# Kernel optimization log

Measured on AMD Instinct MI355X. Metric: run time of the kernel, lower is better.

## Reference

```python
import jax, jax.numpy as jnp
import numpy as np

N = 50000
E = 800000
D_IN = 128
D_OUT = 128


def setup_inputs() -> dict:
    key = jax.random.key(0)
    ks = jax.random.split(key, 12)
    x = jax.random.normal(ks[0], (N, D_IN), dtype=jnp.float32)
    W1 = jax.random.normal(ks[1], (D_IN, D_OUT), dtype=jnp.float32) * (1.0 / np.sqrt(D_IN))
    b1 = jnp.zeros((D_OUT,), dtype=jnp.float32)
    W2 = jax.random.normal(ks[2], (D_IN, D_OUT), dtype=jnp.float32) * (1.0 / np.sqrt(D_IN))
    b2 = jnp.zeros((D_OUT,), dtype=jnp.float32)
    # inverted-dropout masks, p=0.5 -> values in {0, 2}
    def mask(k):
        return jnp.where(jax.random.uniform(k, (N, D_IN)) < 0.5, 0.0, 2.0).astype(jnp.float32)
    mask_pos1 = mask(ks[3])
    mask_neg1 = mask(ks[4])
    mask_pos2 = mask(ks[5])
    mask_neg2 = mask(ks[6])
    edge_index1 = jax.random.randint(ks[7], (2, E), 0, N, dtype=jnp.int32)
    edge_index2 = jax.random.randint(ks[8], (2, E), 0, N, dtype=jnp.int32)
    perm1 = jax.random.permutation(ks[9], N).astype(jnp.int32)
    perm2 = jax.random.permutation(ks[10], N).astype(jnp.int32)
    return dict(x=x, W1=W1, b1=b1, W2=W2, b2=b2,
                mask_pos1=mask_pos1, mask_neg1=mask_neg1,
                mask_pos2=mask_pos2, mask_neg2=mask_neg2,
                edge_index1=edge_index1, edge_index2=edge_index2,
                perm1=perm1, perm2=perm2)


def gcn_conv(x, W, b, edge_index):
    """PyG GCNConv: add self-loops, symmetric normalization, then x@W aggregation + bias."""
    n = x.shape[0]
    xw = x @ W  # [N, D_OUT]
    loops = jnp.arange(n, dtype=edge_index.dtype)
    src = jnp.concatenate([edge_index[0], loops])
    dst = jnp.concatenate([edge_index[1], loops])
    deg = jax.ops.segment_sum(jnp.ones_like(dst, dtype=xw.dtype), dst, num_segments=n)
    dinv = jax.lax.rsqrt(jnp.maximum(deg, 1.0))  # deg >= 1 due to self-loops
    norm = dinv[src] * dinv[dst]                 # [E+N]
    msg = xw[src] * norm[:, None]                # [E+N, D_OUT]
    out = jax.ops.segment_sum(msg, dst, num_segments=n)
    return out + b


def _branch(x, W, b, edge_index, mask_pos, mask_neg, perm):
    pos_h = jax.nn.relu(gcn_conv(x * mask_pos, W, b, edge_index))
    neg_in = (x * mask_neg)[perm]
    neg_h = jax.nn.relu(gcn_conv(neg_in, W, b, edge_index))
    summary = jnp.mean(pos_h, axis=0, keepdims=True)  # [1, D_OUT]
    return pos_h, neg_h, summary


def reference(x, W1, b1, W2, b2, mask_pos1, mask_neg1, mask_pos2, mask_neg2,
              edge_index1, edge_index2, perm1, perm2):
    p1, n1, s1 = _branch(x, W1, b1, edge_index1, mask_pos1, mask_neg1, perm1)
    p2, n2, s2 = _branch(x, W2, b2, edge_index2, mask_pos2, mask_neg2, perm2)
    return (p1, n1, s1, p2, n2, s2)
```

## Files before the change

### kernel.cpp

```cpp
#include <hip/hip_runtime.h>
#include <hip/hip_fp16.h>

#define NN 50000
#define NE 800000
#define D 128
#define NB 196
#define FILL_BLOCKS 1024
#define GEMM_BLOCKS 3128
#define RNG 6250
#define ESL 6250

typedef _Float16 half8_t __attribute__((ext_vector_type(8)));
typedef _Float16 half4_t __attribute__((ext_vector_type(4)));
typedef float f32x4 __attribute__((ext_vector_type(4)));

__global__ void k_init(int* cnt1, int* cnt2, float* s1, float* s2) {
    int i = blockIdx.x * blockDim.x + threadIdx.x;
    int stride = gridDim.x * blockDim.x;
    for (int j = i; j < NN; j += stride) { cnt1[j] = 0; cnt2[j] = 0; }
    if (i < D) { s1[i] = 0.f; s2[i] = 0.f; }
}

__global__ void k_count(const int* __restrict__ dst1, const int* __restrict__ dst2,
                        int* cnt1, int* cnt2) {
    int r = blockIdx.x & 7;
    int rank = blockIdx.x >> 3;
    unsigned lo = r * RNG;
    int base = rank * ESL;
    for (int e = base + threadIdx.x; e < base + ESL; e += 256) {
        int d1 = dst1[e];
        if ((unsigned)(d1 - lo) < RNG) atomicAdd(&cnt1[d1], 1);
        int d2 = dst2[e];
        if ((unsigned)(d2 - lo) < RNG) atomicAdd(&cnt2[d2], 1);
    }
}

__global__ void k_part(const int* __restrict__ cnt1, const int* __restrict__ cnt2,
                       int* part1, int* part2) {
    __shared__ int sm1[256], sm2[256];
    int t = threadIdx.x;
    int idx = blockIdx.x * 256 + t;
    int v1 = (idx < NN) ? cnt1[idx] : 0;
    int v2 = (idx < NN) ? cnt2[idx] : 0;
    sm1[t] = v1; sm2[t] = v2;
    __syncthreads();
    for (int off = 128; off > 0; off >>= 1) {
        if (t < off) { sm1[t] += sm1[t + off]; sm2[t] += sm2[t + off]; }
        __syncthreads();
    }
    if (t == 0) { part1[blockIdx.x] = sm1[0]; part2[blockIdx.x] = sm2[0]; }
}

__global__ void k_scanp(int* part1, int* part2) {
    __shared__ int sm1[256], sm2[256];
    int t = threadIdx.x;
    int v1 = (t < NB) ? part1[t] : 0;
    int v2 = (t < NB) ? part2[t] : 0;
    sm1[t] = v1; sm2[t] = v2;
    __syncthreads();
    for (int off = 1; off < 256; off <<= 1) {
        int a1 = (t >= off) ? sm1[t - off] : 0;
        int a2 = (t >= off) ? sm2[t - off] : 0;
        __syncthreads();
        sm1[t] += a1; sm2[t] += a2;
        __syncthreads();
    }
    if (t < NB) { part1[t] = sm1[t] - v1; part2[t] = sm2[t] - v2; }
}

__global__ void k_apply(const int* __restrict__ cnt1, const int* __restrict__ cnt2,
                        const int* __restrict__ part1, const int* __restrict__ part2,
                        int* rp1, int* rp2, int* cur1, int* cur2,
                        float* dinv1, float* dinv2) {
    __shared__ int sm1[256], sm2[256];
    int b = blockIdx.x, t = threadIdx.x;
    int idx = b * 256 + t;
    int v1 = (idx < NN) ? cnt1[idx] : 0;
    int v2 = (idx < NN) ? cnt2[idx] : 0;
    sm1[t] = v1; sm2[t] = v2;
    __syncthreads();
    for (int off = 1; off < 256; off <<= 1) {
        int a1 = (t >= off) ? sm1[t - off] : 0;
        int a2 = (t >= off) ? sm2[t - off] : 0;
        __syncthreads();
        sm1[t] += a1; sm2[t] += a2;
        __syncthreads();
    }
    int e1 = sm1[t] - v1 + part1[b];
    int e2 = sm2[t] - v2 + part2[b];
    if (idx < NN) {
        rp1[idx] = e1; cur1[idx] = e1; dinv1[idx] = rsqrtf((float)(v1 + 1));
        rp2[idx] = e2; cur2[idx] = e2; dinv2[idx] = rsqrtf((float)(v2 + 1));
    } else if (idx == NN) {
        rp1[NN] = e1; rp2[NN] = e2;
    }
}

__launch_bounds__(256)
__global__ void k_fill_gemm(const int* __restrict__ src1, const int* __restrict__ dst1,
                            const int* __restrict__ src2, const int* __restrict__ dst2,
                            int* cur1, int* cur2, int* col1, int* col2,
                            const float* __restrict__ x,
                            const float* __restrict__ W1, const float* __restrict__ W2,
                            const float* __restrict__ mp1, const float* __restrict__ mn1,
                            const float* __restrict__ mp2, const float* __restrict__ mn2,
                            const int* __restrict__ perm1, const int* __restrict__ perm2,
                            const float* __restrict__ dinv1, const float* __restrict__ dinv2,
                            _Float16* xwi1, _Float16* xwi2) {
    __shared__ __align__(16) _Float16 WT[128][136];
    int t = threadIdx.x;

    if (blockIdx.x < FILL_BLOCKS) {
        int r = blockIdx.x & 7;
        int rank = blockIdx.x >> 3;
        unsigned lo = r * RNG;
        int base = rank * ESL;
        for (int e = base + t; e < base + ESL; e += 256) {
            int d1 = dst1[e];
            if ((unsigned)(d1 - lo) < RNG) {
                int p = atomicAdd(&cur1[d1], 1);
                col1[p] = src1[e];
            }
            int d2 = dst2[e];
            if ((unsigned)(d2 - lo) < RNG) {
                int p = atomicAdd(&cur2[d2], 1);
                col2[p] = src2[e];
            }
        }
        return;
    }

    int g = blockIdx.x - FILL_BLOCKS;
    int which = g / 782;
    int bx = g - which * 782;
    const float* W = (which < 2) ? W1 : W2;
    const float* mask = (which == 0) ? mp1 : (which == 1) ? mn1 : (which == 2) ? mp2 : mn2;
    const int* perm = (which == 1) ? perm1 : (which == 3) ? perm2 : nullptr;
    const float* dinv = (which < 2) ? dinv1 : dinv2;
    _Float16* out = ((which < 2) ? xwi1 : xwi2) + ((which & 1) ? 128 : 0);

    for (int i = 0; i < 16; i++) {
        int idx = i * 256 + t;
        int k = idx >> 5;
        int j4 = (idx & 31) * 4;
        float4 w = ((const float4*)W)[idx];
        WT[j4 + 0][k] = (_Float16)w.x;
        WT[j4 + 1][k] = (_Float16)w.y;
        WT[j4 + 2][k] = (_Float16)w.z;
        WT[j4 + 3][k] = (_Float16)w.w;
    }
    __syncthreads();

    int wave = t >> 6;
    int lane = t & 63;
    int quad = lane >> 4;
    int m = lane & 15;
    int tile = bx * 4 + wave;
    if (tile * 16 >= NN) return;

    int row = tile * 16 + m;
    int grow = perm ? perm[row] : row;
    const float* xrow = x + (long)grow * D;
    const float* mrow = mask + (long)grow * D;

    half8_t a[4];
    for (int kk = 0; kk < 4; kk++) {
        int k0 = kk * 32 + quad * 8;
        float4 xa = *(const float4*)(xrow + k0);
        float4 xb = *(const float4*)(xrow + k0 + 4);
        float4 ma = *(const float4*)(mrow + k0);
        float4 mb = *(const float4*)(mrow + k0 + 4);
        a[kk][0] = (_Float16)(xa.x * ma.x);
        a[kk][1] = (_Float16)(xa.y * ma.y);
        a[kk][2] = (_Float16)(xa.z * ma.z);
        a[kk][3] = (_Float16)(xa.w * ma.w);
        a[kk][4] = (_Float16)(xb.x * mb.x);
        a[kk][5] = (_Float16)(xb.y * mb.y);
        a[kk][6] = (_Float16)(xb.z * mb.z);
        a[kk][7] = (_Float16)(xb.w * mb.w);
    }

    int rbase = tile * 16 + quad * 4;
    float ds0 = dinv[rbase + 0], ds1 = dinv[rbase + 1];
    float ds2 = dinv[rbase + 2], ds3 = dinv[rbase + 3];

    for (int nt = 0; nt < 8; nt++) {
        f32x4 acc = {0.f, 0.f, 0.f, 0.f};
        for (int kk = 0; kk < 4; kk++) {
            half8_t b = *(const half8_t*)(&WT[nt * 16 + m][kk * 32 + quad * 8]);
            acc = __builtin_amdgcn_mfma_f32_16x16x32_f16(a[kk], b, acc, 0, 0, 0);
        }
        int n = nt * 16 + m;
        out[(long)(rbase + 0) * 256 + n] = (_Float16)(acc[0] * ds0);
        out[(long)(rbase + 1) * 256 + n] = (_Float16)(acc[1] * ds1);
        out[(long)(rbase + 2) * 256 + n] = (_Float16)(acc[2] * ds2);
        out[(long)(rbase + 3) * 256 + n] = (_Float16)(acc[3] * ds3);
    }
}

__launch_bounds__(256)
__global__ void k_agg(const _Float16* __restrict__ xwi1, const _Float16* __restrict__ xwi2,
                      const int* __restrict__ rp1, const int* __restrict__ col1,
                      const float* __restrict__ dinv1,
                      const int* __restrict__ rp2, const int* __restrict__ col2,
                      const float* __restrict__ dinv2,
                      const float* __restrict__ b1, const float* __restrict__ b2,
                      float* out) {
    int g = blockIdx.y;
    const _Float16* xwi = g ? xwi2 : xwi1;
    const int* rp = g ? rp2 : rp1;
    const int* col = g ? col2 : col1;
    const float* dinv = g ? dinv2 : dinv1;
    const float* bias = g ? b2 : b1;
    float* pos_out = out + (g ? 12800128L : 0L);
    float* neg_out = out + (g ? 19200128L : 6400000L);

    int t = threadIdx.x;
    int wave = t >> 6, lane = t & 63;
    int i = blockIdx.x * 4 + wave;
    if (i >= NN) return;
    int j4 = lane * 4;

    half4_t sv = *(const half4_t*)(xwi + (long)i * 256 + j4);
    float a0 = (float)sv[0], a1 = (float)sv[1], a2 = (float)sv[2], a3 = (float)sv[3];
    int e0 = rp[i], e1 = rp[i + 1];
    int e = e0;
    for (; e + 8 <= e1; e += 8) {
        int s0 = col[e + 0], s1 = col[e + 1], s2 = col[e + 2], s3 = col[e + 3];
        int s4 = col[e + 4], s5 = col[e + 5], s6 = col[e + 6], s7 = col[e + 7];
        half4_t v0 = *(const half4_t*)(xwi + (long)s0 * 256 + j4);
        half4_t v1 = *(const half4_t*)(xwi + (long)s1 * 256 + j4);
        half4_t v2 = *(const half4_t*)(xwi + (long)s2 * 256 + j4);
        half4_t v3 = *(const half4_t*)(xwi + (long)s3 * 256 + j4);
        half4_t v4 = *(const half4_t*)(xwi + (long)s4 * 256 + j4);
        half4_t v5 = *(const half4_t*)(xwi + (long)s5 * 256 + j4);
        half4_t v6 = *(const half4_t*)(xwi + (long)s6 * 256 + j4);
        half4_t v7 = *(const half4_t*)(xwi + (long)s7 * 256 + j4);
        a0 += (float)v0[0] + (float)v1[0] + (float)v2[0] + (float)v3[0]
            + (float)v4[0] + (float)v5[0] + (float)v6[0] + (float)v7[0];
        a1 += (float)v0[1] + (float)v1[1] + (float)v2[1] + (float)v3[1]
            + (float)v4[1] + (float)v5[1] + (float)v6[1] + (float)v7[1];
        a2 += (float)v0[2] + (float)v1[2] + (float)v2[2] + (float)v3[2]
            + (float)v4[2] + (float)v5[2] + (float)v6[2] + (float)v7[2];
        a3 += (float)v0[3] + (float)v1[3] + (float)v2[3] + (float)v3[3]
            + (float)v4[3] + (float)v5[3] + (float)v6[3] + (float)v7[3];
    }
    for (; e + 4 <= e1; e += 4) {
        int s0 = col[e + 0], s1 = col[e + 1], s2 = col[e + 2], s3 = col[e + 3];
        half4_t v0 = *(const half4_t*)(xwi + (long)s0 * 256 + j4);
        half4_t v1 = *(const half4_t*)(xwi + (long)s1 * 256 + j4);
        half4_t v2 = *(const half4_t*)(xwi + (long)s2 * 256 + j4);
        half4_t v3 = *(const half4_t*)(xwi + (long)s3 * 256 + j4);
        a0 += (float)v0[0] + (float)v1[0] + (float)v2[0] + (float)v3[0];
        a1 += (float)v0[1] + (float)v1[1] + (float)v2[1] + (float)v3[1];
        a2 += (float)v0[2] + (float)v1[2] + (float)v2[2] + (float)v3[2];
        a3 += (float)v0[3] + (float)v1[3] + (float)v2[3] + (float)v3[3];
    }
    for (; e < e1; e++) {
        int s = col[e];
        half4_t v = *(const half4_t*)(xwi + (long)s * 256 + j4);
        a0 += (float)v[0]; a1 += (float)v[1]; a2 += (float)v[2]; a3 += (float)v[3];
    }
    float di = dinv[i];
    int jj = (lane < 32) ? j4 : (j4 - 128);
    const f32x4* bp = (const f32x4*)(bias + jj);
    f32x4 bv = *bp;
    f32x4 o;
    o[0] = fmaxf(0.f, di * a0 + bv[0]);
    o[1] = fmaxf(0.f, di * a1 + bv[1]);
    o[2] = fmaxf(0.f, di * a2 + bv[2]);
    o[3] = fmaxf(0.f, di * a3 + bv[3]);
    float* dst = ((lane < 32) ? pos_out : neg_out) + (long)i * D + jj;
    __builtin_nontemporal_store(o, (f32x4*)dst);
}

__launch_bounds__(256)
__global__ void k_sum(const float* __restrict__ pos1, const float* __restrict__ pos2,
                      float* s1, float* s2) {
    int g = blockIdx.y;
    const float* pos = g ? pos2 : pos1;
    float* s = g ? s2 : s1;
    int t = threadIdx.x;
    int rg = t >> 5;
    int j = (t & 31) * 4;
    float4 acc = {0.f, 0.f, 0.f, 0.f};
    for (int i = blockIdx.x * 8 + rg; i < NN; i += gridDim.x * 8) {
        float4 v = *(const float4*)(pos + (long)i * D + j);
        acc.x += v.x; acc.y += v.y; acc.z += v.z; acc.w += v.w;
    }
    __shared__ float sm[8][128];
    sm[rg][j + 0] = acc.x;
    sm[rg][j + 1] = acc.y;
    sm[rg][j + 2] = acc.z;
    sm[rg][j + 3] = acc.w;
    __syncthreads();
    if (t < 128) {
        float v = 0.f;
        for (int r = 0; r < 8; r++) v += sm[r][t];
        atomicAdd(&s[t], v * (1.0f / NN));
    }
}

extern "C" void kernel_launch(void* const* d_in, const int* in_sizes, int n_in,
                              void* d_out, int out_size, void* d_ws, size_t ws_size,
                              hipStream_t stream) {
    const float* x   = (const float*)d_in[0];
    const float* W1  = (const float*)d_in[1];
    const float* b1  = (const float*)d_in[2];
    const float* W2  = (const float*)d_in[3];
    const float* b2  = (const float*)d_in[4];
    const float* mp1 = (const float*)d_in[5];
    const float* mn1 = (const float*)d_in[6];
    const float* mp2 = (const float*)d_in[7];
    const float* mn2 = (const float*)d_in[8];
    const int* e1 = (const int*)d_in[9];
    const int* e2 = (const int*)d_in[10];
    const int* perm1 = (const int*)d_in[11];
    const int* perm2 = (const int*)d_in[12];
    const int* src1 = e1;       const int* dst1 = e1 + NE;
    const int* src2 = e2;       const int* dst2 = e2 + NE;
    float* out = (float*)d_out;

    char* w = (char*)d_ws;
    _Float16* xwi1 = (_Float16*)w; w += (size_t)NN * 256 * 2;
    _Float16* xwi2 = (_Float16*)w; w += (size_t)NN * 256 * 2;
    int* cnt1 = (int*)w;  w += (size_t)NN * 4;
    int* cnt2 = (int*)w;  w += (size_t)NN * 4;
    int* cur1 = (int*)w;  w += (size_t)NN * 4;
    int* cur2 = (int*)w;  w += (size_t)NN * 4;
    int* rp1 = (int*)w;   w += (size_t)(NN + 4) * 4;
    int* rp2 = (int*)w;   w += (size_t)(NN + 4) * 4;
    int* col1 = (int*)w;  w += (size_t)NE * 4;
    int* col2 = (int*)w;  w += (size_t)NE * 4;
    float* dinv1 = (float*)w; w += (size_t)NN * 4;
    float* dinv2 = (float*)w; w += (size_t)NN * 4;
    int* part1 = (int*)w; w += (size_t)256 * 4;
    int* part2 = (int*)w; w += (size_t)256 * 4;

    float* s1 = out + 12800000L;
    float* s2 = out + 25600128L;
    const float* pos1 = out;
    const float* pos2 = out + 12800128L;

    k_init<<<dim3(256), 256, 0, stream>>>(cnt1, cnt2, s1, s2);
    k_count<<<dim3(1024), 256, 0, stream>>>(dst1, dst2, cnt1, cnt2);
    k_part<<<dim3(NB), 256, 0, stream>>>(cnt1, cnt2, part1, part2);
    k_scanp<<<dim3(1), 256, 0, stream>>>(part1, part2);
    k_apply<<<dim3(NB), 256, 0, stream>>>(cnt1, cnt2, part1, part2,
                                          rp1, rp2, cur1, cur2, dinv1, dinv2);
    k_fill_gemm<<<dim3(FILL_BLOCKS + GEMM_BLOCKS), 256, 0, stream>>>(
        src1, dst1, src2, dst2, cur1, cur2, col1, col2,
        x, W1, W2, mp1, mn1, mp2, mn2, perm1, perm2, dinv1, dinv2, xwi1, xwi2);
    k_agg<<<dim3(12500, 2), 256, 0, stream>>>(xwi1, xwi2,
                                              rp1, col1, dinv1, rp2, col2, dinv2,
                                              b1, b2, out);
    k_sum<<<dim3(128, 2), 256, 0, stream>>>(pos1, pos2, s1, s2);
}
```

Measured before the change: 531.7 us.

## Interleave fill and GEMM blocks; stage GEMM output via LDS for coalesced stores

The fused fill/GEMM kernel now interleaves CSR-fill blocks with GEMM blocks in groups of eight, so the atomic-heavy scatter work overlaps with MFMA work instead of running as a front-loaded phase. The GEMM swaps MFMA operands so each lane holds a row-major output fragment. Results are scaled by dinv, written to shared memory, and then stored to global memory as 16-byte vectors instead of scattered 2-byte stores. The W transpose load is also reworked to write half8 vectors into LDS. This adds an extra __syncthreads and keeps eight accumulator vectors live in registers, which raises register pressure.

```diff
diff --git a/kernel.cpp b/kernel.cpp
--- a/kernel.cpp
+++ b/kernel.cpp
@@ -5,8 +5,7 @@
 #define NE 800000
 #define D 128
 #define NB 196
-#define FILL_BLOCKS 1024
-#define GEMM_BLOCKS 3128
+#define TOT_BLOCKS 4152
 #define RNG 6250
 #define ESL 6250
 
@@ -109,10 +108,12 @@
                             _Float16* xwi1, _Float16* xwi2) {
     __shared__ __align__(16) _Float16 WT[128][136];
     int t = threadIdx.x;
-
-    if (blockIdx.x < FILL_BLOCKS) {
-        int r = blockIdx.x & 7;
-        int rank = blockIdx.x >> 3;
+    int bid = blockIdx.x;
+    int grp = bid >> 3;
+
+    if (((grp & 3) == 0) && (grp < 512)) {
+        int r = bid & 7;
+        int rank = grp >> 2;
         unsigned lo = r * RNG;
         int base = rank * ESL;
         for (int e = base + t; e < base + ESL; e += 256) {
@@ -130,7 +131,7 @@
         return;
     }
 
-    int g = blockIdx.x - FILL_BLOCKS;
+    int g = bid - 8 * min((grp + 3) >> 2, 128);
     int which = g / 782;
     int bx = g - which * 782;
     const float* W = (which < 2) ? W1 : W2;
@@ -139,15 +140,15 @@
     const float* dinv = (which < 2) ? dinv1 : dinv2;
     _Float16* out = ((which < 2) ? xwi1 : xwi2) + ((which & 1) ? 128 : 0);
 
-    for (int i = 0; i < 16; i++) {
+    #pragma unroll
+    for (int i = 0; i < 8; i++) {
         int idx = i * 256 + t;
-        int k = idx >> 5;
-        int j4 = (idx & 31) * 4;
-        float4 w = ((const float4*)W)[idx];
-        WT[j4 + 0][k] = (_Float16)w.x;
-        WT[j4 + 1][k] = (_Float16)w.y;
-        WT[j4 + 2][k] = (_Float16)w.z;
-        WT[j4 + 3][k] = (_Float16)w.w;
+        int j = idx & 127;
+        int k0 = (idx >> 7) * 8;
+        half8_t h;
+        #pragma unroll
+        for (int c = 0; c < 8; c++) h[c] = (_Float16)W[(k0 + c) * 128 + j];
+        *(half8_t*)(&WT[j][k0]) = h;
     }
     __syncthreads();
 
@@ -156,45 +157,67 @@
     int quad = lane >> 4;
     int m = lane & 15;
     int tile = bx * 4 + wave;
-    if (tile * 16 >= NN) return;
-
-    int row = tile * 16 + m;
-    int grow = perm ? perm[row] : row;
-    const float* xrow = x + (long)grow * D;
-    const float* mrow = mask + (long)grow * D;
-
-    half8_t a[4];
-    for (int kk = 0; kk < 4; kk++) {
-        int k0 = kk * 32 + quad * 8;
-        float4 xa = *(const float4*)(xrow + k0);
-        float4 xb = *(const float4*)(xrow + k0 + 4);
-        float4 ma = *(const float4*)(mrow + k0);
-        float4 mb = *(const float4*)(mrow + k0 + 4);
-        a[kk][0] = (_Float16)(xa.x * ma.x);
-        a[kk][1] = (_Float16)(xa.y * ma.y);
-        a[kk][2] = (_Float16)(xa.z * ma.z);
-        a[kk][3] = (_Float16)(xa.w * ma.w);
-        a[kk][4] = (_Float16)(xb.x * mb.x);
-        a[kk][5] = (_Float16)(xb.y * mb.y);
-        a[kk][6] = (_Float16)(xb.z * mb.z);
-        a[kk][7] = (_Float16)(xb.w * mb.w);
-    }
-
-    int rbase = tile * 16 + quad * 4;
-    float ds0 = dinv[rbase + 0], ds1 = dinv[rbase + 1];
-    float ds2 = dinv[rbase + 2], ds3 = dinv[rbase + 3];
-
-    for (int nt = 0; nt < 8; nt++) {
-        f32x4 acc = {0.f, 0.f, 0.f, 0.f};
+    bool active = (tile * 16 < NN);
+
+    f32x4 accs[8];
+    if (active) {
+        int row = tile * 16 + m;
+        int grow = perm ? perm[row] : row;
+        const float* xrow = x + (long)grow * D;
+        const float* mrow = mask + (long)grow * D;
+
+        half8_t a[4];
+        #pragma unroll
         for (int kk = 0; kk < 4; kk++) {
-            half8_t b = *(const half8_t*)(&WT[nt * 16 + m][kk * 32 + quad * 8]);
-            acc = __builtin_amdgcn_mfma_f32_16x16x32_f16(a[kk], b, acc, 0, 0, 0);
-        }
-        int n = nt * 16 + m;
-        out[(long)(rbase + 0) * 256 + n] = (_Float16)(acc[0] * ds0);
-        out[(long)(rbase + 1) * 256 + n] = (_Float16)(acc[1] * ds1);
-        out[(long)(rbase + 2) * 256 + n] = (_Float16)(acc[2] * ds2);
-        out[(long)(rbase + 3) * 256 + n] = (_Float16)(acc[3] * ds3);
+            int k0 = kk * 32 + quad * 8;
+            float4 xa = *(const float4*)(xrow + k0);
+            float4 xb = *(const float4*)(xrow + k0 + 4);
+            float4 ma = *(const float4*)(mrow + k0);
+            float4 mb = *(const float4*)(mrow + k0 + 4);
+            a[kk][0] = (_Float16)(xa.x * ma.x);
+            a[kk][1] = (_Float16)(xa.y * ma.y);
+            a[kk][2] = (_Float16)(xa.z * ma.z);
+            a[kk][3] = (_Float16)(xa.w * ma.w);
+            a[kk][4] = (_Float16)(xb.x * mb.x);
+            a[kk][5] = (_Float16)(xb.y * mb.y);
+            a[kk][6] = (_Float16)(xb.z * mb.z);
+            a[kk][7] = (_Float16)(xb.w * mb.w);
+        }
+
+        #pragma unroll
+        for (int nt = 0; nt < 8; nt++) {
+            f32x4 acc = {0.f, 0.f, 0.f, 0.f};
+            #pragma unroll
+            for (int kk = 0; kk < 4; kk++) {
+                half8_t w = *(const half8_t*)(&WT[nt * 16 + m][kk * 32 + quad * 8]);
+                acc = __builtin_amdgcn_mfma_f32_16x16x32_f16(w, a[kk], acc, 0, 0, 0);
+            }
+            accs[nt] = acc;
+        }
+    }
+
+    __syncthreads();
+
+    if (active) {
+        float ds = dinv[tile * 16 + m];
+        _Float16* st = &WT[0][0] + wave * 2176;
+
+        #pragma unroll
+        for (int nt = 0; nt < 8; nt++) {
+            half4_t h;
+            h[0] = (_Float16)(accs[nt][0] * ds);
+            h[1] = (_Float16)(accs[nt][1] * ds);
+            h[2] = (_Float16)(accs[nt][2] * ds);
+            h[3] = (_Float16)(accs[nt][3] * ds);
+            *(half4_t*)(st + m * 136 + nt * 16 + quad * 4) = h;
+        }
+        #pragma unroll
+        for (int p = 0; p < 4; p++) {
+            int r = lane & 15;
+            int cc = (lane >> 4) + p * 4;
+            half8_t v = *(const half8_t*)(st + r * 136 + cc * 8);
+            *(half8_t*)(out + (long)(tile * 16 + r) * 256 + cc * 8) = v;
+        }
     }
 }
 
@@ -348,7 +371,7 @@
     k_scanp<<<dim3(1), 256, 0, stream>>>(part1, part2);
     k_apply<<<dim3(NB), 256, 0, stream>>>(cnt1, cnt2, part1, part2,
                                           rp1, rp2, cur1, cur2, dinv1, dinv2);
-    k_fill_gemm<<<dim3(FILL_BLOCKS + GEMM_BLOCKS), 256, 0, stream>>>(
+    k_fill_gemm<<<dim3(TOT_BLOCKS), 256, 0, stream>>>(
         src1, dst1, src2, dst2, cur1, cur2, col1, col2,
         x, W1, W2, mp1, mn1, mp2, mn2, perm1, perm2, dinv1, dinv2, xwi1, xwi2);
     k_agg<<<dim3(12500, 2), 256, 0, stream>>>(xwi1, xwi2,
```

Result: slower. 637.2 us (+19.8%).
